# Optimization experiments

Hardware: AMD Instinct MI355X
Metric: run time of the kernel (lower is better)

The kernel has to match this reference:

```python
import jax, jax.numpy as jnp
import numpy as np

N, E, G = 100000, 600000, 2000
CONV = [128, 256, 256, 256]
LIN = [256, 128, 1]
BN_EPS = 1e-5


def setup_inputs() -> dict:
    key = jax.random.key(0)
    ks = iter(jax.random.split(key, 64))
    inp = {}
    inp["x"] = jax.random.normal(next(ks), (N, CONV[0]), dtype=jnp.float32)
    inp["edge_index"] = jax.random.randint(next(ks), (2, E), 0, N)
    inp["batch"] = jnp.sort(jax.random.randint(next(ks), (N,), 0, G))

    def lin_w(k, i, o):
        return (jax.random.normal(k, (i, o), dtype=jnp.float32) / np.sqrt(i)).astype(jnp.float32)

    # 3 GINConv MLPs: Linear(in,out), BN(out), ReLU, Linear(out,out), ReLU
    for i in range(3):
        ci, co = CONV[i], CONV[i + 1]
        inp[f"c{i}_w1"] = lin_w(next(ks), ci, co)
        inp[f"c{i}_b1"] = jnp.zeros((co,), jnp.float32)
        inp[f"c{i}_g"] = jnp.ones((co,), jnp.float32)
        inp[f"c{i}_be"] = jnp.zeros((co,), jnp.float32)
        inp[f"c{i}_m"] = jax.random.normal(next(ks), (co,), dtype=jnp.float32) * 0.1
        inp[f"c{i}_v"] = jax.random.uniform(next(ks), (co,), minval=0.5, maxval=1.5, dtype=jnp.float32)
        inp[f"c{i}_w2"] = lin_w(next(ks), co, co)
        inp[f"c{i}_b2"] = jnp.zeros((co,), jnp.float32)
    # head: Linear(256,128) + BN(128) + ReLU, Linear(128,1)
    inp["l0_w"] = lin_w(next(ks), LIN[0], LIN[1])
    inp["l0_b"] = jnp.zeros((LIN[1],), jnp.float32)
    inp["l0_g"] = jnp.ones((LIN[1],), jnp.float32)
    inp["l0_be"] = jnp.zeros((LIN[1],), jnp.float32)
    inp["l0_m"] = jax.random.normal(next(ks), (LIN[1],), dtype=jnp.float32) * 0.1
    inp["l0_v"] = jax.random.uniform(next(ks), (LIN[1],), minval=0.5, maxval=1.5, dtype=jnp.float32)
    inp["l1_w"] = lin_w(next(ks), LIN[1], LIN[2])
    inp["l1_b"] = jnp.zeros((LIN[2],), jnp.float32)
    return inp


def _bn(h, g, be, m, v):
    return g * (h - m) * jax.lax.rsqrt(v + BN_EPS) + be


def _gin_conv(x, src, dst, w1, b1, g, be, m, v, w2, b2):
    # GINConv (eps=0): MLP(x + sum_{j in N(i)} x_j); messages x[src] aggregated at dst
    agg = jax.ops.segment_sum(x[src], dst, num_segments=x.shape[0])
    h = (x + agg) @ w1 + b1
    h = jax.nn.relu(_bn(h, g, be, m, v))
    return jax.nn.relu(h @ w2 + b2)


def reference(x, edge_index, batch,
              c0_w1, c0_b1, c0_g, c0_be, c0_m, c0_v, c0_w2, c0_b2,
              c1_w1, c1_b1, c1_g, c1_be, c1_m, c1_v, c1_w2, c1_b2,
              c2_w1, c2_b1, c2_g, c2_be, c2_m, c2_v, c2_w2, c2_b2,
              l0_w, l0_b, l0_g, l0_be, l0_m, l0_v, l1_w, l1_b):
    src, dst = edge_index[0], edge_index[1]
    conv_params = [
        (c0_w1, c0_b1, c0_g, c0_be, c0_m, c0_v, c0_w2, c0_b2),
        (c1_w1, c1_b1, c1_g, c1_be, c1_m, c1_v, c1_w2, c1_b2),
        (c2_w1, c2_b1, c2_g, c2_be, c2_m, c2_v, c2_w2, c2_b2),
    ]
    h = x
    for i, p in enumerate(conv_params):
        h = _gin_conv(h, src, dst, *p)
        if i < 2:
            h = jax.nn.relu(h)  # outer activation (no-op after ReLU, kept for fidelity)
    # global_add_pool over graphs
    h = jax.ops.segment_sum(h, batch, num_segments=G)  # [G, 256]
    h = h @ l0_w + l0_b
    h = _bn(h, l0_g, l0_be, l0_m, l0_v)
    h = jax.nn.relu(h)  # dropout is identity in eval mode
    return h @ l1_w + l1_b  # [G, 1]
```

## Files before the change

### kernel.cpp

```cpp
#include <hip/hip_runtime.h>
#include <hip/hip_bf16.h>

#define BN_EPS 1e-5f

typedef __attribute__((ext_vector_type(8))) short short8;
typedef __attribute__((ext_vector_type(4))) float f32x4;

__device__ __forceinline__ void gll16(const void* g, void* l) {
    __builtin_amdgcn_global_load_lds(
        (const __attribute__((address_space(1))) unsigned int*)g,
        (__attribute__((address_space(3))) unsigned int*)l, 16, 0, 0);
}

__device__ __forceinline__ unsigned pack_bf2(float a, float b) {
    __hip_bfloat16 ba = __float2bfloat16(a);
    __hip_bfloat16 bb = __float2bfloat16(b);
    return (unsigned)(*(unsigned short*)&ba) | ((unsigned)(*(unsigned short*)&bb) << 16);
}

__global__ void hist_kernel(const int* __restrict__ dst, int* __restrict__ off, int E) {
    int e = blockIdx.x * blockDim.x + threadIdx.x;
    if (e < E) atomicAdd(&off[dst[e] + 1], 1);
}

__global__ __launch_bounds__(256) void scan1_kernel(int* __restrict__ data,
                                                    int* __restrict__ sums, int n) {
    __shared__ int sh[256];
    const int t = threadIdx.x;
    const int idx = blockIdx.x * 1024 + t * 4;
    int v[4];
    int s = 0;
#pragma unroll
    for (int j = 0; j < 4; ++j) {
        int x = (idx + j < n) ? data[idx + j] : 0;
        s += x;
        v[j] = s;
    }
    sh[t] = s;
    __syncthreads();
    for (int o = 1; o < 256; o <<= 1) {
        int x = (t >= o) ? sh[t - o] : 0;
        __syncthreads();
        sh[t] += x;
        __syncthreads();
    }
    const int prev = sh[t] - s;
#pragma unroll
    for (int j = 0; j < 4; ++j) {
        if (idx + j < n) data[idx + j] = v[j] + prev;
    }
    if (t == 255) sums[blockIdx.x] = sh[255];
}

__global__ __launch_bounds__(256) void scan2_kernel(int* __restrict__ sums, int nb) {
    __shared__ int sh[256];
    const int t = threadIdx.x;
    sh[t] = (t < nb) ? sums[t] : 0;
    __syncthreads();
    for (int o = 1; o < 256; o <<= 1) {
        int x = (t >= o) ? sh[t - o] : 0;
        __syncthreads();
        sh[t] += x;
        __syncthreads();
    }
    if (t < nb) sums[t] = sh[t];
}

__global__ void scan3_kernel(int* __restrict__ data, const int* __restrict__ sums,
                             int* __restrict__ cursor, int n, int N) {
    int i = blockIdx.x * blockDim.x + threadIdx.x;
    if (i >= n) return;
    int b = i >> 10;
    int v = data[i];
    if (b > 0) { v += sums[b - 1]; data[i] = v; }
    if (i < N) cursor[i] = v;
}

__global__ void fill_kernel(const int* __restrict__ src, const int* __restrict__ dst,
                            int* __restrict__ cursor, int* __restrict__ sorted_src, int E) {
    int e = blockIdx.x * blockDim.x + threadIdx.x;
    if (e >= E) return;
    int p = atomicAdd(&cursor[dst[e]], 1);
    sorted_src[p] = src[e];
}

__global__ void cvt_x_kernel(const float* __restrict__ x, __hip_bfloat16* __restrict__ xb,
                             int N, int total4 ) {
    int i = blockIdx.x * blockDim.x + threadIdx.x;
    if (i >= total4) return;
    int n = i >> 5;
    unsigned lo = 0, hi = 0;
    if (n < N) {
        const float4 v = ((const float4*)x)[i];
        lo = pack_bf2(v.x, v.y);
        hi = pack_bf2(v.z, v.w);
    }
    ((uint2*)xb)[i] = make_uint2(lo, hi);
}

__global__ void wt_all_kernel(const float* __restrict__ w0, const float* __restrict__ w1,
                              const float* __restrict__ w2, const float* __restrict__ w3,
                              const float* __restrict__ w4, const float* __restrict__ w5,
                              __hip_bfloat16* __restrict__ o0, __hip_bfloat16* __restrict__ o1,
                              __hip_bfloat16* __restrict__ o2, __hip_bfloat16* __restrict__ o3,
                              __hip_bfloat16* __restrict__ o4, __hip_bfloat16* __restrict__ o5) {
    int i = blockIdx.x * blockDim.x + threadIdx.x;
    const int S0 = 256 * 128, S = 256 * 256;
    if (i < S0) {
        int m = i / 128, k = i - m * 128;
        o0[i] = __float2bfloat16(w0[k * 256 + m]);
        return;
    }
    i -= S0;
    int mi = i / S, j = i - mi * S;
    if (mi >= 5) return;
    int m = j >> 8, k = j & 255;
    const float* Wp; __hip_bfloat16* Op;
    switch (mi) {
        case 0: Wp = w1; Op = o1; break;
        case 1: Wp = w2; Op = o2; break;
        case 2: Wp = w3; Op = o3; break;
        case 3: Wp = w4; Op = o4; break;
        default: Wp = w5; Op = o5; break;
    }
    Op[j] = __float2bfloat16(Wp[k * 256 + m]);
}

__global__ void prep_ss_kernel(
    const float* __restrict__ g0, const float* __restrict__ be0, const float* __restrict__ m0,
    const float* __restrict__ v0, const float* __restrict__ b10, const float* __restrict__ b20,
    const float* __restrict__ g1, const float* __restrict__ be1, const float* __restrict__ m1,
    const float* __restrict__ v1, const float* __restrict__ b11, const float* __restrict__ b21,
    const float* __restrict__ g2, const float* __restrict__ be2, const float* __restrict__ m2,
    const float* __restrict__ v2, const float* __restrict__ b12, const float* __restrict__ b22,
    float* __restrict__ ss) {
    const int layer = blockIdx.x;
    const int c = threadIdx.x;
    const float *g, *be, *m, *v, *b1, *b2;
    switch (layer) {
        case 0: g = g0; be = be0; m = m0; v = v0; b1 = b10; b2 = b20; break;
        case 1: g = g1; be = be1; m = m1; v = v1; b1 = b11; b2 = b21; break;
        default: g = g2; be = be2; m = m2; v = v2; b1 = b12; b2 = b22; break;
    }
    float r = rsqrtf(v[c] + BN_EPS);
    float s = g[c] * r;
    ss[(2 * layer) * 512 + c] = s;
    ss[(2 * layer) * 512 + 256 + c] = (b1[c] - m[c]) * s + be[c];
    ss[(2 * layer + 1) * 512 + c] = 1.f;
    ss[(2 * layer + 1) * 512 + 256 + c] = b2[c];
}

template <int C>
__global__ __launch_bounds__(256) void agg_fused(const __hip_bfloat16* __restrict__ h,
                                                 const int* __restrict__ off,
                                                 const int* __restrict__ ssrc,
                                                 __hip_bfloat16* __restrict__ out, int N) {
    constexpr int L = C / 8;
    int t = blockIdx.x * blockDim.x + threadIdx.x;
    int n = t / L;
    if (n >= N) return;
    int c8 = t - n * L;
    const uint4* hp = (const uint4*)h;

    float acc[8];
    {
        uint4 sv = hp[(size_t)n * L + c8];
        const unsigned u[4] = {sv.x, sv.y, sv.z, sv.w};
#pragma unroll
        for (int j = 0; j < 4; ++j) {
            acc[2 * j]     = __uint_as_float(u[j] << 16);
            acc[2 * j + 1] = __uint_as_float(u[j] & 0xffff0000u);
        }
    }
    const int e0 = off[n], e1 = off[n + 1];
    int e = e0;
    for (; e + 2 <= e1; e += 2) {
        int s0 = ssrc[e], s1 = ssrc[e + 1];
        uint4 a = hp[(size_t)s0 * L + c8];
        uint4 b = hp[(size_t)s1 * L + c8];
        const unsigned ua[4] = {a.x, a.y, a.z, a.w};
        const unsigned ub[4] = {b.x, b.y, b.z, b.w};
#pragma unroll
        for (int j = 0; j < 4; ++j) {
            acc[2 * j]     += __uint_as_float(ua[j] << 16);
            acc[2 * j + 1] += __uint_as_float(ua[j] & 0xffff0000u);
            acc[2 * j]     += __uint_as_float(ub[j] << 16);
            acc[2 * j + 1] += __uint_as_float(ub[j] & 0xffff0000u);
        }
    }
    if (e < e1) {
        int s0 = ssrc[e];
        uint4 a = hp[(size_t)s0 * L + c8];
        const unsigned ua[4] = {a.x, a.y, a.z, a.w};
#pragma unroll
        for (int j = 0; j < 4; ++j) {
            acc[2 * j]     += __uint_as_float(ua[j] << 16);
            acc[2 * j + 1] += __uint_as_float(ua[j] & 0xffff0000u);
        }
    }
    unsigned o[4];
#pragma unroll
    for (int j = 0; j < 4; ++j) o[j] = pack_bf2(acc[2 * j], acc[2 * j + 1]);
    ((uint4*)out)[(size_t)n * L + c8] = make_uint4(o[0], o[1], o[2], o[3]);
}

template <int K1>
__global__ __launch_bounds__(512, 4) void mlp_fused(
    const __hip_bfloat16* __restrict__ A,
    const __hip_bfloat16* __restrict__ W1t,
    const __hip_bfloat16* __restrict__ W2t,
    const float* __restrict__ ss1, const float* __restrict__ ss2,
    __hip_bfloat16* __restrict__ C) {
    __shared__ __align__(16) char bufT[64 * 1024];

    const int tid = threadIdx.x;
    const int l   = tid & 63;
    const int w   = tid >> 6;
    const int l15 = l & 15;
    const int kg  = l >> 4;
    const size_t row0 = (size_t)blockIdx.x * 128;

    constexpr int ROWB = K1 * 2;
    constexpr int NT1  = K1 / 32;

    const char* W1base = (const char*)W1t + (size_t)(w * 32 + l15) * ROWB + kg * 16;
    const char* W2base = (const char*)W2t + (size_t)(w * 32 + l15) * 512 + kg * 16;

    short8 wc0 = *(const short8*)(W1base);
    short8 wc1 = *(const short8*)(W1base + 16 * ROWB);

    {
        const char* Ab = (const char*)(A + row0 * K1);
#pragma unroll
        for (int ib = w; ib < 8 * NT1; ib += 8) {
            const int j = ib / NT1, t = ib % NT1;
            gll16(Ab + (size_t)(j * 16 + l15) * ROWB + t * 64 + kg * 16,
                  bufT + ib * 1024);
        }
    }
    asm volatile("s_waitcnt vmcnt(0)" ::: "memory");
    __syncthreads();

    f32x4 acc[2][8];
#pragma unroll
    for (int i = 0; i < 2; ++i)
#pragma unroll
        for (int j = 0; j < 8; ++j) acc[i][j] = (f32x4){0.f, 0.f, 0.f, 0.f};

    {
        auto step = [&](int t, short8 wa, short8 wb) {
#pragma unroll
            for (int jh = 0; jh < 2; ++jh) {
                short8 af[4];
#pragma unroll
                for (int jj = 0; jj < 4; ++jj)
                    af[jj] = *(const short8*)(bufT + ((jh * 4 + jj) * NT1 + t) * 1024 + l * 16);
#pragma unroll
                for (int jj = 0; jj < 4; ++jj) {
                    acc[0][jh * 4 + jj] = __builtin_amdgcn_mfma_f32_16x16x32_bf16(
                        wa, af[jj], acc[0][jh * 4 + jj], 0, 0, 0);
                    acc[1][jh * 4 + jj] = __builtin_amdgcn_mfma_f32_16x16x32_bf16(
                        wb, af[jj], acc[1][jh * 4 + jj], 0, 0, 0);
                }
            }
        };
#pragma unroll 1
        for (int t = 0; t < NT1 - 1; ++t) {
            short8 wn0 = *(const short8*)(W1base + (t + 1) * 64);
            short8 wn1 = *(const short8*)(W1base + 16 * ROWB + (t + 1) * 64);
            step(t, wc0, wc1);
            wc0 = wn0; wc1 = wn1;
        }
        step(NT1 - 1, wc0, wc1);
    }
    __syncthreads();

    wc0 = *(const short8*)(W2base);
    wc1 = *(const short8*)(W2base + 16 * 512);

#pragma unroll
    for (int i = 0; i < 2; ++i) {
        const int m0 = w * 32 + i * 16 + kg * 4;
        const float4 s4 = *(const float4*)(ss1 + m0);
        const float4 h4 = *(const float4*)(ss1 + 256 + m0);
        const int toff = w * 1024 + (i * 2 + (kg >> 1)) * 256 + l15 * 16 + (kg & 1) * 8;
#pragma unroll
        for (int j = 0; j < 8; ++j) {
            const float v0 = fmaxf(acc[i][j][0] * s4.x + h4.x, 0.f);
            const float v1 = fmaxf(acc[i][j][1] * s4.y + h4.y, 0.f);
            const float v2 = fmaxf(acc[i][j][2] * s4.z + h4.z, 0.f);
            const float v3 = fmaxf(acc[i][j][3] * s4.w + h4.w, 0.f);
            *(uint2*)(bufT + j * 8192 + toff) = make_uint2(pack_bf2(v0, v1), pack_bf2(v2, v3));
        }
    }
    __syncthreads();

#pragma unroll
    for (int i = 0; i < 2; ++i)
#pragma unroll
        for (int j = 0; j < 8; ++j) acc[i][j] = (f32x4){0.f, 0.f, 0.f, 0.f};

    {
        auto step = [&](int t, short8 wa, short8 wb) {
#pragma unroll
            for (int jh = 0; jh < 2; ++jh) {
                short8 tf[4];
#pragma unroll
                for (int jj = 0; jj < 4; ++jj)
                    tf[jj] = *(const short8*)(bufT + ((jh * 4 + jj) * 8 + t) * 1024 + l * 16);
#pragma unroll
                for (int jj = 0; jj < 4; ++jj) {
                    acc[0][jh * 4 + jj] = __builtin_amdgcn_mfma_f32_16x16x32_bf16(
                        wa, tf[jj], acc[0][jh * 4 + jj], 0, 0, 0);
                    acc[1][jh * 4 + jj] = __builtin_amdgcn_mfma_f32_16x16x32_bf16(
                        wb, tf[jj], acc[1][jh * 4 + jj], 0, 0, 0);
                }
            }
        };
#pragma unroll 1
        for (int t = 0; t < 7; ++t) {
            short8 wn0 = *(const short8*)(W2base + (t + 1) * 64);
            short8 wn1 = *(const short8*)(W2base + 16 * 512 + (t + 1) * 64);
            step(t, wc0, wc1);
            wc0 = wn0; wc1 = wn1;
        }
        step(7, wc0, wc1);
    }
    __syncthreads();

#pragma unroll
    for (int i = 0; i < 2; ++i) {
        const int c0 = w * 32 + i * 16 + kg * 4;
        const float4 s4 = *(const float4*)(ss2 + c0);
        const float4 h4 = *(const float4*)(ss2 + 256 + c0);
        const int toff = w * 1024 + (i * 2 + (kg >> 1)) * 256 + l15 * 16 + (kg & 1) * 8;
#pragma unroll
        for (int j = 0; j < 8; ++j) {
            const float v0 = fmaxf(acc[i][j][0] * s4.x + h4.x, 0.f);
            const float v1 = fmaxf(acc[i][j][1] * s4.y + h4.y, 0.f);
            const float v2 = fmaxf(acc[i][j][2] * s4.z + h4.z, 0.f);
            const float v3 = fmaxf(acc[i][j][3] * s4.w + h4.w, 0.f);
            *(uint2*)(bufT + j * 8192 + toff) = make_uint2(pack_bf2(v0, v1), pack_bf2(v2, v3));
        }
    }
    __syncthreads();

    {
        char* Cb = (char*)C + row0 * 512;
#pragma unroll
        for (int q = tid; q < 4096; q += 512) {
            const int j  = q >> 9;
            const int wp = (q >> 6) & 7;
            const int lp = q & 63;
            uint4 v = *(const uint4*)(bufT + q * 16);
            *(uint4*)(Cb + (size_t)(j * 16 + (lp & 15)) * 512 + wp * 64 + (lp >> 4) * 16) = v;
        }
    }
}

__device__ __forceinline__ int lower_bound_dev(const int* __restrict__ a, int n, int key) {
    int lo = 0, hi = n;
    while (lo < hi) {
        int mid = (lo + hi) >> 1;
        if (a[mid] < key) lo = mid + 1; else hi = mid;
    }
    return lo;
}

__global__ __launch_bounds__(256) void pool_seg_kernel(const __hip_bfloat16* __restrict__ h,
                                                       const int* __restrict__ batch,
                                                       float* __restrict__ pooled, int N) {
    __shared__ int seg[2];
    const int g = blockIdx.x;
    if (threadIdx.x == 0) seg[0] = lower_bound_dev(batch, N, g);
    if (threadIdx.x == 1) seg[1] = lower_bound_dev(batch, N, g + 1);
    __syncthreads();
    const int c = threadIdx.x;
    float acc = 0.f;
    for (int n = seg[0]; n < seg[1]; ++n) acc += __bfloat162float(h[(size_t)n * 256 + c]);
    pooled[(size_t)g * 256 + c] = acc;
}

__global__ __launch_bounds__(128) void head_kernel(
    const float* __restrict__ pooled,
    const float* __restrict__ w0, const float* __restrict__ b0,
    const float* __restrict__ g, const float* __restrict__ be,
    const float* __restrict__ m, const float* __restrict__ v,
    const float* __restrict__ w1, const float* __restrict__ b1,
    float* __restrict__ out) {
    __shared__ float row[256];
    __shared__ float red[128];
    const int gid = blockIdx.x;
    const int j = threadIdx.x;

    row[j]       = pooled[(size_t)gid * 256 + j];
    row[j + 128] = pooled[(size_t)gid * 256 + 128 + j];
    __syncthreads();

    float acc = b0[j];
#pragma unroll 8
    for (int k = 0; k < 256; ++k) acc += row[k] * w0[k * 128 + j];

    float h = g[j] * (acc - m[j]) * rsqrtf(v[j] + BN_EPS) + be[j];
    h = fmaxf(h, 0.f) * w1[j];
    red[j] = h;
    __syncthreads();
    for (int s = 64; s > 0; s >>= 1) {
        if (j < s) red[j] += red[j + s];
        __syncthreads();
    }
    if (j == 0) out[gid] = red[0] + b1[0];
}

extern "C" void kernel_launch(void* const* d_in, const int* in_sizes, int n_in,
                              void* d_out, int out_size, void* d_ws, size_t ws_size,
                              hipStream_t stream) {
    const float* x    = (const float*)d_in[0];
    const int* eidx   = (const int*)d_in[1];
    const int* batch  = (const int*)d_in[2];

    const int N = in_sizes[0] / 128;
    const int E = in_sizes[1] / 2;
    const int G = out_size;

    const int* src = eidx;
    const int* dst = eidx + E;

    const float* cw1[3]; const float* cb1[3]; const float* cg[3]; const float* cbe[3];
    const float* cm[3];  const float* cv[3];  const float* cw2[3]; const float* cb2[3];
    for (int i = 0; i < 3; ++i) {
        int b = 3 + i * 8;
        cw1[i] = (const float*)d_in[b + 0];
        cb1[i] = (const float*)d_in[b + 1];
        cg[i]  = (const float*)d_in[b + 2];
        cbe[i] = (const float*)d_in[b + 3];
        cm[i]  = (const float*)d_in[b + 4];
        cv[i]  = (const float*)d_in[b + 5];
        cw2[i] = (const float*)d_in[b + 6];
        cb2[i] = (const float*)d_in[b + 7];
    }
    const float* l0_w  = (const float*)d_in[27];
    const float* l0_b  = (const float*)d_in[28];
    const float* l0_g  = (const float*)d_in[29];
    const float* l0_be = (const float*)d_in[30];
    const float* l0_m  = (const float*)d_in[31];
    const float* l0_v  = (const float*)d_in[32];
    const float* l1_w  = (const float*)d_in[33];
    const float* l1_b  = (const float*)d_in[34];

    float* outp = (float*)d_out;

    const int nrb  = (N + 127) / 128;
    const int Npad = nrb * 128;
    const size_t SB = (size_t)Npad * 256 * 2;
    const size_t XB = (size_t)Npad * 128 * 2;
    const size_t PB = (size_t)G * 256 * 4;
    const size_t WTB = (size_t)256 * 256 * 2;

    char* ws = (char*)d_ws;
    size_t o = 0;
    __hip_bfloat16* U  = (__hip_bfloat16*)(ws + o); o += SB;
    __hip_bfloat16* V  = (__hip_bfloat16*)(ws + o); o += SB;
    __hip_bfloat16* xb = (__hip_bfloat16*)(ws + o); o += XB;
    float* pooled      = (float*)(ws + o);       o += PB;
    __hip_bfloat16* wt[6];
    for (int i = 0; i < 6; ++i) { wt[i] = (__hip_bfloat16*)(ws + o); o += WTB; }
    float* ss          = (float*)(ws + o);       o += 6 * 512 * 4;
    int* csr_off    = (int*)(ws + o); o += (size_t)(N + 1) * 4;
    int* cursor     = (int*)(ws + o); o += (size_t)N * 4;
    int* sorted_src = (int*)(ws + o); o += (size_t)E * 4;
    int* sums       = (int*)(ws + o); o += 256 * 4;
    if (ws_size < o) return;

    const dim3 blk(256);

    {
        int total4 = Npad * 128 / 4;
        cvt_x_kernel<<<(total4 + 255) / 256, blk, 0, stream>>>(x, xb, N, total4);
    }
    {
        int total = 256 * 128 + 5 * 256 * 256;
        wt_all_kernel<<<(total + 255) / 256, blk, 0, stream>>>(
            cw1[0], cw2[0], cw1[1], cw2[1], cw1[2], cw2[2],
            wt[0], wt[1], wt[2], wt[3], wt[4], wt[5]);
    }
    prep_ss_kernel<<<3, blk, 0, stream>>>(
        cg[0], cbe[0], cm[0], cv[0], cb1[0], cb2[0],
        cg[1], cbe[1], cm[1], cv[1], cb1[1], cb2[1],
        cg[2], cbe[2], cm[2], cv[2], cb1[2], cb2[2], ss);

    {
        const int n_off = N + 1;
        hipMemsetAsync(csr_off, 0, (size_t)n_off * sizeof(int), stream);
        hist_kernel<<<(E + 255) / 256, blk, 0, stream>>>(dst, csr_off, E);
        const int nb = (n_off + 1023) / 1024;
        scan1_kernel<<<nb, blk, 0, stream>>>(csr_off, sums, n_off);
        scan2_kernel<<<1, blk, 0, stream>>>(sums, nb);
        scan3_kernel<<<(n_off + 255) / 256, blk, 0, stream>>>(csr_off, sums, cursor, n_off, N);
        fill_kernel<<<(E + 255) / 256, blk, 0, stream>>>(src, dst, cursor, sorted_src, E);
    }

    auto SS = [&](int i) { return ss + i * 512; };

    {
        int total = N * 16;
        agg_fused<128><<<(total + 255) / 256, blk, 0, stream>>>(xb, csr_off, sorted_src, U, N);
    }
    mlp_fused<128><<<nrb, dim3(512), 0, stream>>>(U, wt[0], wt[1], SS(0), SS(1), V);

    {
        int total = N * 32;
        agg_fused<256><<<(total + 255) / 256, blk, 0, stream>>>(V, csr_off, sorted_src, U, N);
    }
    mlp_fused<256><<<nrb, dim3(512), 0, stream>>>(U, wt[2], wt[3], SS(2), SS(3), U);

    {
        int total = N * 32;
        agg_fused<256><<<(total + 255) / 256, blk, 0, stream>>>(U, csr_off, sorted_src, V, N);
    }
    mlp_fused<256><<<nrb, dim3(512), 0, stream>>>(V, wt[4], wt[5], SS(4), SS(5), V);

    pool_seg_kernel<<<G, blk, 0, stream>>>(V, batch, pooled, N);
    head_kernel<<<G, dim3(128), 0, stream>>>(pooled, l0_w, l0_b, l0_g, l0_be, l0_m, l0_v,
                                             l1_w, l1_b, outp);
}
```

Baseline: 409.4 us.

## Fuse neighbor aggregation into the GIN MLP kernel via LDS staging

Removes the separate agg_fused kernel. Each MLP block now gathers and sums the neighbor bf16 features for its own 128 rows and writes them straight into the swizzled LDS tile the MFMA loop reads. This cuts one launch per layer and the write and read of the aggregated intermediate through global memory. In exchange, the irregular gather now runs inside a 512-thread, LDS-heavy block with lower occupancy, and it no longer overlaps with the async global_load_lds path. Buffer aliasing also changes (layer 2 writes to U and layer 3 reads U), so the gathers must still see consistent inputs.

```diff
diff --git a/kernel.cpp b/kernel.cpp
--- a/kernel.cpp
+++ b/kernel.cpp
@@ -5,12 +5,6 @@
 
 typedef __attribute__((ext_vector_type(8))) short short8;
 typedef __attribute__((ext_vector_type(4))) float f32x4;
-
-__device__ __forceinline__ void gll16(const void* g, void* l) {
-    __builtin_amdgcn_global_load_lds(
-        (const __attribute__((address_space(1))) unsigned int*)g,
-        (__attribute__((address_space(3))) unsigned int*)l, 16, 0, 0);
-}
 
 __device__ __forceinline__ unsigned pack_bf2(float a, float b) {
     __hip_bfloat16 ba = __float2bfloat16(a);
@@ -150,67 +144,14 @@
     ss[(2 * layer + 1) * 512 + 256 + c] = b2[c];
 }
 
-template <int C>
-__global__ __launch_bounds__(256) void agg_fused(const __hip_bfloat16* __restrict__ h,
-                                                 const int* __restrict__ off,
-                                                 const int* __restrict__ ssrc,
-                                                 __hip_bfloat16* __restrict__ out, int N) {
-    constexpr int L = C / 8;
-    int t = blockIdx.x * blockDim.x + threadIdx.x;
-    int n = t / L;
-    if (n >= N) return;
-    int c8 = t - n * L;
-    const uint4* hp = (const uint4*)h;
-
-    float acc[8];
-    {
-        uint4 sv = hp[(size_t)n * L + c8];
-        const unsigned u[4] = {sv.x, sv.y, sv.z, sv.w};
-#pragma unroll
-        for (int j = 0; j < 4; ++j) {
-            acc[2 * j]     = __uint_as_float(u[j] << 16);
-            acc[2 * j + 1] = __uint_as_float(u[j] & 0xffff0000u);
-        }
-    }
-    const int e0 = off[n], e1 = off[n + 1];
-    int e = e0;
-    for (; e + 2 <= e1; e += 2) {
-        int s0 = ssrc[e], s1 = ssrc[e + 1];
-        uint4 a = hp[(size_t)s0 * L + c8];
-        uint4 b = hp[(size_t)s1 * L + c8];
-        const unsigned ua[4] = {a.x, a.y, a.z, a.w};
-        const unsigned ub[4] = {b.x, b.y, b.z, b.w};
-#pragma unroll
-        for (int j = 0; j < 4; ++j) {
-            acc[2 * j]     += __uint_as_float(ua[j] << 16);
-            acc[2 * j + 1] += __uint_as_float(ua[j] & 0xffff0000u);
-            acc[2 * j]     += __uint_as_float(ub[j] << 16);
-            acc[2 * j + 1] += __uint_as_float(ub[j] & 0xffff0000u);
-        }
-    }
-    if (e < e1) {
-        int s0 = ssrc[e];
-        uint4 a = hp[(size_t)s0 * L + c8];
-        const unsigned ua[4] = {a.x, a.y, a.z, a.w};
-#pragma unroll
-        for (int j = 0; j < 4; ++j) {
-            acc[2 * j]     += __uint_as_float(ua[j] << 16);
-            acc[2 * j + 1] += __uint_as_float(ua[j] & 0xffff0000u);
-        }
-    }
-    unsigned o[4];
-#pragma unroll
-    for (int j = 0; j < 4; ++j) o[j] = pack_bf2(acc[2 * j], acc[2 * j + 1]);
-    ((uint4*)out)[(size_t)n * L + c8] = make_uint4(o[0], o[1], o[2], o[3]);
-}
-
 template <int K1>
-__global__ __launch_bounds__(512, 4) void mlp_fused(
-    const __hip_bfloat16* __restrict__ A,
+__global__ __launch_bounds__(512, 4) void mlp_agg_fused(
+    const __hip_bfloat16* __restrict__ H,
+    const int* __restrict__ off, const int* __restrict__ ssrc,
     const __hip_bfloat16* __restrict__ W1t,
     const __hip_bfloat16* __restrict__ W2t,
     const float* __restrict__ ss1, const float* __restrict__ ss2,
-    __hip_bfloat16* __restrict__ C) {
+    __hip_bfloat16* __restrict__ C, int N) {
     __shared__ __align__(16) char bufT[64 * 1024];
 
     const int tid = threadIdx.x;
@@ -222,23 +163,72 @@
 
     constexpr int ROWB = K1 * 2;
     constexpr int NT1  = K1 / 32;
+    constexpr int CH   = K1 / 8;
+    constexpr int RPW  = 64 / CH;
+    constexpr int LCH  = (K1 == 256) ? 5 : 4;
 
     const char* W1base = (const char*)W1t + (size_t)(w * 32 + l15) * ROWB + kg * 16;
     const char* W2base = (const char*)W2t + (size_t)(w * 32 + l15) * 512 + kg * 16;
-
     short8 wc0 = *(const short8*)(W1base);
     short8 wc1 = *(const short8*)(W1base + 16 * ROWB);
 
     {
-        const char* Ab = (const char*)(A + row0 * K1);
-#pragma unroll
-        for (int ib = w; ib < 8 * NT1; ib += 8) {
-            const int j = ib / NT1, t = ib % NT1;
-            gll16(Ab + (size_t)(j * 16 + l15) * ROWB + t * 64 + kg * 16,
-                  bufT + ib * 1024);
+        const uint4* hp = (const uint4*)H;
+#pragma unroll 1
+        for (int pass = 0; pass < 16 / RPW; ++pass) {
+            const int rg = pass * RPW + (l >> LCH);
+            const int craw = l & (CH - 1);
+            const int c = (craw & ~3) | ((craw ^ rg) & 3);
+            const int r = (int)row0 + w * 16 + rg;
+
+            float acc[8];
+#pragma unroll
+            for (int j = 0; j < 8; ++j) acc[j] = 0.f;
+
+            if (r < N) {
+                {
+                    uint4 sv = hp[(size_t)r * CH + c];
+                    const unsigned u[4] = {sv.x, sv.y, sv.z, sv.w};
+#pragma unroll
+                    for (int j = 0; j < 4; ++j) {
+                        acc[2 * j]     = __uint_as_float(u[j] << 16);
+                        acc[2 * j + 1] = __uint_as_float(u[j] & 0xffff0000u);
+                    }
+                }
+                const int e0 = off[r], e1 = off[r + 1];
+                int e = e0;
+                for (; e + 2 <= e1; e += 2) {
+                    int s0 = ssrc[e], s1 = ssrc[e + 1];
+                    uint4 a = hp[(size_t)s0 * CH + c];
+                    uint4 b = hp[(size_t)s1 * CH + c];
+                    const unsigned ua[4] = {a.x, a.y, a.z, a.w};
+                    const unsigned ub[4] = {b.x, b.y, b.z, b.w};
+#pragma unroll
+                    for (int j = 0; j < 4; ++j) {
+                        acc[2 * j]     += __uint_as_float(ua[j] << 16);
+                        acc[2 * j + 1] += __uint_as_float(ua[j] & 0xffff0000u);
+                        acc[2 * j]     += __uint_as_float(ub[j] << 16);
+                        acc[2 * j + 1] += __uint_as_float(ub[j] & 0xffff0000u);
+                    }
+                }
+                if (e < e1) {
+                    int s0 = ssrc[e];
+                    uint4 a = hp[(size_t)s0 * CH + c];
+                    const unsigned ua[4] = {a.x, a.y, a.z, a.w};
+#pragma unroll
+                    for (int j = 0; j < 4; ++j) {
+                        acc[2 * j]     += __uint_as_float(ua[j] << 16);
+                        acc[2 * j + 1] += __uint_as_float(ua[j] & 0xffff0000u);
+                    }
+                }
+            }
+            const int ib = w * NT1 + (c >> 2);
+            const int slot = (c & 3) * 16 + rg;
+            uint4 ov = make_uint4(pack_bf2(acc[0], acc[1]), pack_bf2(acc[2], acc[3]),
+                                  pack_bf2(acc[4], acc[5]), pack_bf2(acc[6], acc[7]));
+            *(uint4*)(bufT + (size_t)ib * 1024 + slot * 16) = ov;
         }
     }
-    asm volatile("s_waitcnt vmcnt(0)" ::: "memory");
     __syncthreads();
 
     f32x4 acc[2][8];
@@ -502,23 +492,12 @@
 
     auto SS = [&](int i) { return ss + i * 512; };
 
-    {
-        int total = N * 16;
-        agg_fused<128><<<(total + 255) / 256, blk, 0, stream>>>(xb, csr_off, sorted_src, U, N);
-    }
-    mlp_fused<128><<<nrb, dim3(512), 0, stream>>>(U, wt[0], wt[1], SS(0), SS(1), V);
-
-    {
-        int total = N * 32;
-        agg_fused<256><<<(total + 255) / 256, blk, 0, stream>>>(V, csr_off, sorted_src, U, N);
-    }
-    mlp_fused<256><<<nrb, dim3(512), 0, stream>>>(U, wt[2], wt[3], SS(2), SS(3), U);
-
-    {
-        int total = N * 32;
-        agg_fused<256><<<(total + 255) / 256, blk, 0, stream>>>(U, csr_off, sorted_src, V, N);
-    }
-    mlp_fused<256><<<nrb, dim3(512), 0, stream>>>(V, wt[4], wt[5], SS(4), SS(5), V);
+    mlp_agg_fused<128><<<nrb, dim3(512), 0, stream>>>(
+        xb, csr_off, sorted_src, wt[0], wt[1], SS(0), SS(1), V, N);
+    mlp_agg_fused<256><<<nrb, dim3(512), 0, stream>>>(
+        V, csr_off, sorted_src, wt[2], wt[3], SS(2), SS(3), U, N);
+    mlp_agg_fused<256><<<nrb, dim3(512), 0, stream>>>(
+        U, csr_off, sorted_src, wt[4], wt[5], SS(4), SS(5), V, N);
 
     pool_seg_kernel<<<G, blk, 0, stream>>>(V, batch, pooled, N);
     head_kernel<<<G, dim3(128), 0, stream>>>(pooled, l0_w, l0_b, l0_g, l0_be, l0_m, l0_v,
```

Measured after the change: 413.8 us. Within noise of the previous version (+1.1%).

## Fuse global add pooling into last MLP epilogue and unroll aggregation by four

Applied to the files above, without the earlier changes.

The last GIN MLP kernel now pools its output rows straight from shared memory into per-graph sums with atomic adds. This removes the separate pool kernel and the write and re-read of the final activations. Pooled sums are now taken from the bf16-rounded values before any global store, and the atomics make the order of float additions nondeterministic. The edge aggregation loop also gains a 4-way unrolled path that issues more independent gathers per iteration.

```diff
diff --git a/kernel.cpp b/kernel.cpp
--- a/kernel.cpp
+++ b/kernel.cpp
@@ -174,6 +174,24 @@
     }
     const int e0 = off[n], e1 = off[n + 1];
     int e = e0;
+    for (; e + 4 <= e1; e += 4) {
+        int s0 = ssrc[e], s1 = ssrc[e + 1], s2 = ssrc[e + 2], s3 = ssrc[e + 3];
+        uint4 a = hp[(size_t)s0 * L + c8];
+        uint4 b = hp[(size_t)s1 * L + c8];
+        uint4 cc = hp[(size_t)s2 * L + c8];
+        uint4 d = hp[(size_t)s3 * L + c8];
+        const unsigned ua[4] = {a.x, a.y, a.z, a.w};
+        const unsigned ub[4] = {b.x, b.y, b.z, b.w};
+        const unsigned uc[4] = {cc.x, cc.y, cc.z, cc.w};
+        const unsigned ud[4] = {d.x, d.y, d.z, d.w};
+#pragma unroll
+        for (int j = 0; j < 4; ++j) {
+            acc[2 * j]     += __uint_as_float(ua[j] << 16) + __uint_as_float(ub[j] << 16) +
+                              __uint_as_float(uc[j] << 16) + __uint_as_float(ud[j] << 16);
+            acc[2 * j + 1] += __uint_as_float(ua[j] & 0xffff0000u) + __uint_as_float(ub[j] & 0xffff0000u) +
+                              __uint_as_float(uc[j] & 0xffff0000u) + __uint_as_float(ud[j] & 0xffff0000u);
+        }
+    }
     for (; e + 2 <= e1; e += 2) {
         int s0 = ssrc[e], s1 = ssrc[e + 1];
         uint4 a = hp[(size_t)s0 * L + c8];
@@ -182,10 +200,8 @@
         const unsigned ub[4] = {b.x, b.y, b.z, b.w};
 #pragma unroll
         for (int j = 0; j < 4; ++j) {
-            acc[2 * j]     += __uint_as_float(ua[j] << 16);
-            acc[2 * j + 1] += __uint_as_float(ua[j] & 0xffff0000u);
-            acc[2 * j]     += __uint_as_float(ub[j] << 16);
-            acc[2 * j + 1] += __uint_as_float(ub[j] & 0xffff0000u);
+            acc[2 * j]     += __uint_as_float(ua[j] << 16) + __uint_as_float(ub[j] << 16);
+            acc[2 * j + 1] += __uint_as_float(ua[j] & 0xffff0000u) + __uint_as_float(ub[j] & 0xffff0000u);
         }
     }
     if (e < e1) {
@@ -204,14 +220,16 @@
     ((uint4*)out)[(size_t)n * L + c8] = make_uint4(o[0], o[1], o[2], o[3]);
 }
 
-template <int K1>
+template <int K1, bool POOL>
 __global__ __launch_bounds__(512, 4) void mlp_fused(
     const __hip_bfloat16* __restrict__ A,
     const __hip_bfloat16* __restrict__ W1t,
     const __hip_bfloat16* __restrict__ W2t,
     const float* __restrict__ ss1, const float* __restrict__ ss2,
-    __hip_bfloat16* __restrict__ C) {
+    __hip_bfloat16* __restrict__ C,
+    const int* __restrict__ batch, float* __restrict__ pooled, int N) {
     __shared__ __align__(16) char bufT[64 * 1024];
+    __shared__ int batch_sh[128];
 
     const int tid = threadIdx.x;
     const int l   = tid & 63;
@@ -343,9 +361,13 @@
             *(uint2*)(bufT + j * 8192 + toff) = make_uint2(pack_bf2(v0, v1), pack_bf2(v2, v3));
         }
     }
-    __syncthreads();
-
-    {
+    if (POOL && tid < 128) {
+        const int r = (int)row0 + tid;
+        batch_sh[tid] = (r < N) ? batch[r] : -1;
+    }
+    __syncthreads();
+
+    if (!POOL) {
         char* Cb = (char*)C + row0 * 512;
 #pragma unroll
         for (int q = tid; q < 4096; q += 512) {
@@ -355,30 +377,28 @@
             uint4 v = *(const uint4*)(bufT + q * 16);
             *(uint4*)(Cb + (size_t)(j * 16 + (lp & 15)) * 512 + wp * 64 + (lp >> 4) * 16) = v;
         }
-    }
-}
-
-__device__ __forceinline__ int lower_bound_dev(const int* __restrict__ a, int n, int key) {
-    int lo = 0, hi = n;
-    while (lo < hi) {
-        int mid = (lo + hi) >> 1;
-        if (a[mid] < key) lo = mid + 1; else hi = mid;
-    }
-    return lo;
-}
-
-__global__ __launch_bounds__(256) void pool_seg_kernel(const __hip_bfloat16* __restrict__ h,
-                                                       const int* __restrict__ batch,
-                                                       float* __restrict__ pooled, int N) {
-    __shared__ int seg[2];
-    const int g = blockIdx.x;
-    if (threadIdx.x == 0) seg[0] = lower_bound_dev(batch, N, g);
-    if (threadIdx.x == 1) seg[1] = lower_bound_dev(batch, N, g + 1);
-    __syncthreads();
-    const int c = threadIdx.x;
-    float acc = 0.f;
-    for (int n = seg[0]; n < seg[1]; ++n) acc += __bfloat162float(h[(size_t)n * 256 + c]);
-    pooled[(size_t)g * 256 + c] = acc;
+    } else {
+        const int c  = tid & 255;
+        const int rh = tid >> 8;
+        const int cbase = (c >> 5) * 1024 +
+                          (((c >> 4) & 1) * 2 + ((c >> 3) & 1)) * 256 +
+                          ((c >> 2) & 1) * 8 + (c & 3) * 2;
+        float accp = 0.f;
+        int gprev = -1;
+        for (int nn = rh * 64; nn < rh * 64 + 64; ++nn) {
+            const int g = batch_sh[nn];
+            if (g < 0) break;
+            if (g != gprev) {
+                if (gprev >= 0) atomicAdd(&pooled[(size_t)gprev * 256 + c], accp);
+                accp = 0.f;
+                gprev = g;
+            }
+            const unsigned short* p =
+                (const unsigned short*)(bufT + (nn >> 4) * 8192 + cbase + (nn & 15) * 16);
+            accp += __uint_as_float(((unsigned)*p) << 16);
+        }
+        if (gprev >= 0) atomicAdd(&pooled[(size_t)gprev * 256 + c], accp);
+    }
 }
 
 __global__ __launch_bounds__(128) void head_kernel(
@@ -474,6 +494,7 @@
 
     const dim3 blk(256);
 
+    hipMemsetAsync(pooled, 0, PB, stream);
     {
         int total4 = Npad * 128 / 4;
         cvt_x_kernel<<<(total4 + 255) / 256, blk, 0, stream>>>(x, xb, N, total4);
@@ -506,21 +527,23 @@
         int total = N * 16;
         agg_fused<128><<<(total + 255) / 256, blk, 0, stream>>>(xb, csr_off, sorted_src, U, N);
     }
-    mlp_fused<128><<<nrb, dim3(512), 0, stream>>>(U, wt[0], wt[1], SS(0), SS(1), V);
+    mlp_fused<128, false><<<nrb, dim3(512), 0, stream>>>(
+        U, wt[0], wt[1], SS(0), SS(1), V, nullptr, nullptr, N);
 
     {
         int total = N * 32;
         agg_fused<256><<<(total + 255) / 256, blk, 0, stream>>>(V, csr_off, sorted_src, U, N);
     }
-    mlp_fused<256><<<nrb, dim3(512), 0, stream>>>(U, wt[2], wt[3], SS(2), SS(3), U);
+    mlp_fused<256, false><<<nrb, dim3(512), 0, stream>>>(
+        U, wt[2], wt[3], SS(2), SS(3), U, nullptr, nullptr, N);
 
     {
         int total = N * 32;
         agg_fused<256><<<(total + 255) / 256, blk, 0, stream>>>(U, csr_off, sorted_src, V, N);
     }
-    mlp_fused<256><<<nrb, dim3(512), 0, stream>>>(V, wt[4], wt[5], SS(4), SS(5), V);
-
-    pool_seg_kernel<<<G, blk, 0, stream>>>(V, batch, pooled, N);
+    mlp_fused<256, true><<<nrb, dim3(512), 0, stream>>>(
+        V, wt[4], wt[5], SS(4), SS(5), nullptr, batch, pooled, N);
+
     head_kernel<<<G, dim3(128), 0, stream>>>(pooled, l0_w, l0_b, l0_g, l0_be, l0_m, l0_v,
                                              l1_w, l1_b, outp);
 }
```

After: 395.6 us. -3.4%, faster.
